# Optimization experiments

Measured on AMD Instinct MI355X. Metric: run time of the kernel, lower is better.

## Reference

```python
import jax, jax.numpy as jnp
import numpy as np

B, S, D = 4, 1024, 1024
H = 16
HD = D // H  # 64
NPOS = 64


def setup_inputs() -> dict:
    key = jax.random.key(0)
    ks = jax.random.split(key, 12)
    f = lambda k, shape, s=0.02: jax.random.normal(k, shape, dtype=jnp.float32) * s
    return {
        "q": jax.random.normal(ks[0], (B, S, D), dtype=jnp.float32),
        "k": jax.random.normal(ks[1], (B, S, D), dtype=jnp.float32),
        "v": jax.random.normal(ks[2], (B, S, D), dtype=jnp.float32),
        "Wq_w": f(ks[3], (D, D)), "Wq_b": f(ks[4], (D,)),
        "Wk_w": f(ks[5], (D, D)), "Wk_b": f(ks[6], (D,)),
        "Wv_w": f(ks[7], (D, D)), "Wv_b": f(ks[8], (D,)),
        "Wo_w": f(ks[9], (D, D)), "Wo_b": f(ks[10], (D,)),
        "pos_emb": f(ks[11], (HD, NPOS)),  # torch param is [1,1,head_dim,npos_max]
    }


def _proj(x, w, b):
    # nn.Linear: x @ w.T + b, then split heads -> [B, H, S, HD]
    y = jnp.einsum("bsd,ed->bse", x, w) + b
    bsz, s, _ = y.shape
    return y.reshape(bsz, s, H, HD).transpose(0, 2, 1, 3)


def reference(q, k, v, Wq_w, Wq_b, Wk_w, Wk_b, Wv_w, Wv_b, Wo_w, Wo_b, pos_emb):
    Q = _proj(q, Wq_w, Wq_b)
    K = _proj(k, Wk_w, Wk_b)
    V = _proj(v, Wv_w, Wv_b)

    scale = 1.0 / np.sqrt(HD).astype(np.float32)
    logits = jnp.einsum("bhqd,bhkd->bhqk", Q, K) * scale  # [B,H,S,S]

    # CoPE: sigmoid gates -> reverse cumsum -> interpolated position-logit gather
    gates = jax.nn.sigmoid(logits)
    pos = jnp.flip(jnp.cumsum(jnp.flip(gates, axis=-1), axis=-1), axis=-1)
    pos = jnp.minimum(pos, NPOS - 1)
    pos_floor = jnp.floor(pos)
    pos_ceil = jnp.ceil(pos)
    logits_int = jnp.einsum("bhqd,dn->bhqn", Q, pos_emb)  # [B,H,S,NPOS]
    lc = jnp.take_along_axis(logits_int, pos_ceil.astype(jnp.int32), axis=-1)
    lf = jnp.take_along_axis(logits_int, pos_floor.astype(jnp.int32), axis=-1)
    w = pos - pos_floor
    logits = logits + lc * w + lf * (1.0 - w)

    score = jax.nn.softmax(logits, axis=-1)
    out = jnp.einsum("bhqk,bhkd->bhqd", score, V)
    out = out.transpose(0, 2, 1, 3).reshape(q.shape[0], q.shape[1], D)
    return jnp.einsum("bsd,ed->bse", out, Wo_w) + Wo_b
```

## Files before the change

kernel.cpp:

```cpp
#include <hip/hip_runtime.h>
#include <hip/hip_bf16.h>

typedef __attribute__((ext_vector_type(8))) short short8;
typedef __attribute__((ext_vector_type(4))) short short4v;
typedef __attribute__((ext_vector_type(4))) float f32x4;
typedef unsigned short us;

#define MFMA16(a,b,c) __builtin_amdgcn_mfma_f32_16x16x32_bf16((a),(b),(c),0,0,0)

static __device__ __forceinline__ us bf16r(float x){
  unsigned u = __builtin_bit_cast(unsigned, x);
  u = u + 0x7fffu + ((u >> 16) & 1u);
  return (us)(u >> 16);
}
static __device__ __forceinline__ unsigned pk2(float a, float b){
  return (unsigned)bf16r(a) | ((unsigned)bf16r(b) << 16);
}

__global__ __launch_bounds__(256)
void castf2b(const float* __restrict__ in, us* __restrict__ out, int n){
  const int i = (blockIdx.x * 256 + threadIdx.x) * 4;
  if (i < n){
    const float4 v = *(const float4*)(in + i);
    short4v o;
    o[0] = (short)bf16r(v.x); o[1] = (short)bf16r(v.y);
    o[2] = (short)bf16r(v.z); o[3] = (short)bf16r(v.w);
    *(short4v*)(out + i) = o;
  }
}

__global__ __launch_bounds__(256)
void transpose_pe(const float* __restrict__ pe, us* __restrict__ peT){
  const int t = threadIdx.x;
  const int n = t & 63, dq = t >> 6;
#pragma unroll
  for (int j = 0; j < 16; ++j){
    const int d = dq * 16 + j;
    peT[n * 64 + d] = bf16r(pe[d * 64 + n]);
  }
}

__global__ __launch_bounds__(256)
void transpose_v(const us* __restrict__ Vb, us* __restrict__ VT){
  __shared__ __align__(16) us tile[64 * 72];
  const int t = threadIdx.x;
  const int stile = blockIdx.x & 15;
  const int bh = blockIdx.x >> 4;
  const int b = bh >> 4, h = bh & 15;
  const int s0 = stile << 6;
#pragma unroll
  for (int c = 0; c < 2; ++c){
    const int idx = t + (c << 8);
    const int sr = idx >> 3, cw = idx & 7;
    *(short8*)&tile[sr * 72 + cw * 8] =
        *(const short8*)(Vb + ((size_t)(b * 1024 + s0 + sr)) * 1024 + h * 64 + cw * 8);
  }
  __syncthreads();
#pragma unroll
  for (int c = 0; c < 2; ++c){
    const int idx = t + (c << 8);
    const int dr = idx >> 3, sw = idx & 7;
    short8 o;
#pragma unroll
    for (int j = 0; j < 8; ++j) o[j] = (short)tile[(sw * 8 + j) * 72 + dr];
    *(short8*)(VT + ((size_t)(bh * 64 + dr)) * 1024 + s0 + sw * 8) = o;
  }
}

template<bool OUT_BF16>
__global__ __launch_bounds__(256)
void gemm3_nt(const us* __restrict__ A0, const us* __restrict__ A1, const us* __restrict__ A2,
              const us* __restrict__ W0, const us* __restrict__ W1, const us* __restrict__ W2,
              const float* __restrict__ bp0, const float* __restrict__ bp1, const float* __restrict__ bp2,
              void* __restrict__ O0, void* __restrict__ O1, void* __restrict__ O2){
  __shared__ __align__(16) us Al[128 * 64];
  __shared__ __align__(16) us Bl[128 * 64];
  const int sel = blockIdx.y;
  const us* A      = sel == 0 ? A0 : (sel == 1 ? A1 : A2);
  const us* Wm     = sel == 0 ? W0 : (sel == 1 ? W1 : W2);
  const float* bias = sel == 0 ? bp0 : (sel == 1 ? bp1 : bp2);
  void* Ov         = sel == 0 ? O0 : (sel == 1 ? O1 : O2);
  const int tid = threadIdx.x;
  const int bm = blockIdx.x & 31, bn = blockIdx.x >> 5;
  const int m0 = bm << 7, n0 = bn << 7;
  const int w = tid >> 6, l = tid & 63;
  const int lr = l & 15, lg = l >> 4;
  const int wm = (w & 1) << 6, wn = (w >> 1) << 6;
  int srow[4], scol[4], sdst[4];
#pragma unroll
  for (int c = 0; c < 4; ++c){
    const int idx = tid + (c << 8);
    const int r = idx >> 3, cw = idx & 7;
    srow[c] = r; scol[c] = cw << 3;
    sdst[c] = r * 64 + ((cw << 3) ^ ((r & 7) << 3));
  }
  const int swz = (lr & 7) << 3;
  f32x4 acc[4][4];
#pragma unroll
  for (int i = 0; i < 4; ++i)
#pragma unroll
    for (int j = 0; j < 4; ++j) acc[i][j] = (f32x4){0.f, 0.f, 0.f, 0.f};

  short8 av[4], bv[4];
#pragma unroll
  for (int c = 0; c < 4; ++c){
    av[c] = *(const short8*)(A  + (size_t)(m0 + srow[c]) * 1024 + scol[c]);
    bv[c] = *(const short8*)(Wm + (size_t)(n0 + srow[c]) * 1024 + scol[c]);
  }
  for (int k0 = 0; k0 < 1024; k0 += 64){
    __syncthreads();
#pragma unroll
    for (int c = 0; c < 4; ++c){
      *(short8*)&Al[sdst[c]] = av[c];
      *(short8*)&Bl[sdst[c]] = bv[c];
    }
    __syncthreads();
    if (k0 < 960){
#pragma unroll
      for (int c = 0; c < 4; ++c){
        av[c] = *(const short8*)(A  + (size_t)(m0 + srow[c]) * 1024 + k0 + 64 + scol[c]);
        bv[c] = *(const short8*)(Wm + (size_t)(n0 + srow[c]) * 1024 + k0 + 64 + scol[c]);
      }
    }
#pragma unroll
    for (int ks = 0; ks < 2; ++ks){
      short8 af[4], bfv[4];
#pragma unroll
      for (int mt = 0; mt < 4; ++mt)
        af[mt] = *(const short8*)&Al[(wm + mt * 16 + lr) * 64 + (((ks << 5) + (lg << 3)) ^ swz)];
#pragma unroll
      for (int nt = 0; nt < 4; ++nt)
        bfv[nt] = *(const short8*)&Bl[(wn + nt * 16 + lr) * 64 + (((ks << 5) + (lg << 3)) ^ swz)];
#pragma unroll
      for (int mt = 0; mt < 4; ++mt)
#pragma unroll
        for (int nt = 0; nt < 4; ++nt)
          acc[mt][nt] = MFMA16(af[mt], bfv[nt], acc[mt][nt]);
    }
  }
  float bb[4];
#pragma unroll
  for (int nt = 0; nt < 4; ++nt) bb[nt] = bias[n0 + wn + nt * 16 + lr];
#pragma unroll
  for (int mt = 0; mt < 4; ++mt)
#pragma unroll
    for (int nt = 0; nt < 4; ++nt)
#pragma unroll
      for (int r = 0; r < 4; ++r){
        const size_t m = m0 + wm + mt * 16 + lg * 4 + r;
        const size_t n = n0 + wn + nt * 16 + lr;
        const float vv = acc[mt][nt][r] + bb[nt];
        if (OUT_BF16) ((us*)Ov)[m * 1024 + n] = bf16r(vv);
        else          ((float*)Ov)[m * 1024 + n] = vv;
      }
}

__global__ __launch_bounds__(256)
void cope_attn_mfma(const us* __restrict__ Qb, const us* __restrict__ Kb,
                    const us* __restrict__ VT, const us* __restrict__ peT,
                    us* __restrict__ Ob){
  __shared__ __align__(16) char smem[16 * 1028 * 4];
  __shared__ float li[16][68];
  float* logl = (float*)smem;
  const int tid = threadIdx.x;
  const int w = tid >> 6, l = tid & 63;
  const int lr = l & 15, lg = l >> 4;
  const int qt = blockIdx.x & 63;
  const int bh = blockIdx.x >> 6;
  const int b = bh >> 4, h = bh & 15;
  const int q0 = qt << 4;
  const us* Qh = Qb + ((size_t)(b * 1024 + q0)) * 1024 + h * 64;
  const us* Kh = Kb + ((size_t)(b * 1024)) * 1024 + h * 64;
  const us* Vh = VT + ((size_t)bh) * 64 * 1024;

  const short8 aq0 = *(const short8*)(Qh + (size_t)lr * 1024 + lg * 8);
  const short8 aq1 = *(const short8*)(Qh + (size_t)lr * 1024 + 32 + lg * 8);

  {
    f32x4 a = (f32x4){0.f, 0.f, 0.f, 0.f};
    const short8 p0 = *(const short8*)(peT + (size_t)(w * 16 + lr) * 64 + lg * 8);
    const short8 p1 = *(const short8*)(peT + (size_t)(w * 16 + lr) * 64 + 32 + lg * 8);
    a = MFMA16(aq0, p0, a);
    a = MFMA16(aq1, p1, a);
#pragma unroll
    for (int r = 0; r < 4; ++r) li[lg * 4 + r][w * 16 + lr] = a[r];
  }
  {
    const int kbase = w << 8;
    const us* Kw = Kh + (size_t)(kbase + lr) * 1024 + lg * 8;
    short8 b0 = *(const short8*)(Kw);
    short8 b1 = *(const short8*)(Kw + 32);
    for (int t = 0; t < 16; ++t){
      short8 n0v = b0, n1v = b1;
      if (t < 15){
        const us* Kn = Kw + (size_t)((t + 1) * 16) * 1024;
        n0v = *(const short8*)(Kn);
        n1v = *(const short8*)(Kn + 32);
      }
      f32x4 a = (f32x4){0.f, 0.f, 0.f, 0.f};
      a = MFMA16(aq0, b0, a);
      a = MFMA16(aq1, b1, a);
      const int kc = kbase + t * 16 + lr;
#pragma unroll
      for (int r = 0; r < 4; ++r) logl[(lg * 4 + r) * 1028 + kc] = a[r] * 0.125f;
      b0 = n0v; b1 = n1v;
    }
  }
  __syncthreads();
  unsigned pp[4][8];
#pragma unroll
  for (int rr = 0; rr < 4; ++rr){
    const int row = w * 4 + rr;
    const float* rowp = logl + row * 1028;
    f32x4 xv[4];
#pragma unroll
    for (int cb = 0; cb < 4; ++cb) xv[cb] = *(const f32x4*)(rowp + cb * 256 + l * 4);
    float s[4], pref[4][4];
#pragma unroll
    for (int cb = 0; cb < 4; ++cb){
      float run = 0.f;
#pragma unroll
      for (int j = 0; j < 4; ++j){
        const float g = 1.f / (1.f + __expf(-xv[cb][j]));
        pref[cb][j] = run;
        run += g;
      }
      s[cb] = run;
    }
    float T[4], lex[4];
#pragma unroll
    for (int cb = 0; cb < 4; ++cb){
      float run = s[cb];
#pragma unroll
      for (int off = 1; off < 64; off <<= 1){
        const float t2 = __shfl_up(run, off);
        if (l >= off) run += t2;
      }
      T[cb] = __shfl(run, 63);
      lex[cb] = run - s[cb];
    }
    float tt = 0.f, pb[4];
#pragma unroll
    for (int cb = 3; cb >= 0; --cb){ pb[cb] = tt + T[cb] - lex[cb]; tt += T[cb]; }
    float mx = -3.4e38f;
#pragma unroll
    for (int cb = 0; cb < 4; ++cb){
#pragma unroll
      for (int j = 0; j < 4; ++j){
        float p = pb[cb] - pref[cb][j];
        p = fminf(p, 63.f);
        p = fmaxf(p, 0.f);
        const float pf = floorf(p);
        const int il = (int)pf;
        const int ic = (int)ceilf(p);
        const float wt = p - pf;
        const float xx = xv[cb][j] + li[row][ic] * wt + li[row][il] * (1.f - wt);
        xv[cb][j] = xx;
        mx = fmaxf(mx, xx);
      }
    }
#pragma unroll
    for (int off = 1; off < 64; off <<= 1) mx = fmaxf(mx, __shfl_xor(mx, off));
    float sum = 0.f;
#pragma unroll
    for (int cb = 0; cb < 4; ++cb)
#pragma unroll
      for (int j = 0; j < 4; ++j){ const float e = __expf(xv[cb][j] - mx); xv[cb][j] = e; sum += e; }
#pragma unroll
    for (int off = 1; off < 64; off <<= 1) sum += __shfl_xor(sum, off);
    const float inv = 1.f / sum;
#pragma unroll
    for (int cb = 0; cb < 4; ++cb){
      pp[rr][cb * 2 + 0] = pk2(xv[cb][0] * inv, xv[cb][1] * inv);
      pp[rr][cb * 2 + 1] = pk2(xv[cb][2] * inv, xv[cb][3] * inv);
    }
  }
  __syncthreads();
  char* Pb = smem + 32768;
#pragma unroll
  for (int rr = 0; rr < 4; ++rr){
    const int row = w * 4 + rr;
#pragma unroll
    for (int cb = 0; cb < 4; ++cb){
      const int off = row * 2048 + ((cb * 512 + l * 8) ^ ((row & 7) << 4));
      uint2 vv; vv.x = pp[rr][cb * 2]; vv.y = pp[rr][cb * 2 + 1];
      *(uint2*)(Pb + off) = vv;
    }
  }
  __syncthreads();
  {
    const int d0 = w * 16;
    const int pswz = (lr & 7) << 4;
    f32x4 a = (f32x4){0.f, 0.f, 0.f, 0.f};
    const us* Vw = Vh + (size_t)(d0 + lr) * 1024 + lg * 8;
    short8 vb = *(const short8*)(Vw);
    for (int ks = 0; ks < 32; ++ks){
      short8 vn = vb;
      if (ks < 31) vn = *(const short8*)(Vw + (ks + 1) * 32);
      const short8 pa = *(const short8*)(Pb + lr * 2048 + (((ks << 6) + (lg << 4)) ^ pswz));
      a = MFMA16(pa, vb, a);
      vb = vn;
    }
#pragma unroll
    for (int r = 0; r < 4; ++r)
      Ob[((size_t)(b * 1024 + q0 + lg * 4 + r)) * 1024 + h * 64 + d0 + lr] = bf16r(a[r]);
  }
}

extern "C" void kernel_launch(void* const* d_in, const int* in_sizes, int n_in,
                              void* d_out, int out_size, void* d_ws, size_t ws_size,
                              hipStream_t stream) {
  const float* q    = (const float*)d_in[0];
  const float* k    = (const float*)d_in[1];
  const float* v    = (const float*)d_in[2];
  const float* Wq_w = (const float*)d_in[3];
  const float* Wq_b = (const float*)d_in[4];
  const float* Wk_w = (const float*)d_in[5];
  const float* Wk_b = (const float*)d_in[6];
  const float* Wv_w = (const float*)d_in[7];
  const float* Wv_b = (const float*)d_in[8];
  const float* Wo_w = (const float*)d_in[9];
  const float* Wo_b = (const float*)d_in[10];
  const float* pe   = (const float*)d_in[11];
  float* out = (float*)d_out;

  char* W = (char*)d_ws;
  const size_t MB = (size_t)1 << 20;
  us* qbf  = (us*)(W);
  us* kbf  = (us*)(W + 8 * MB);
  us* vbf  = (us*)(W + 16 * MB);
  us* Wqb  = (us*)(W + 24 * MB);
  us* Wkb  = (us*)(W + 26 * MB);
  us* Wvb  = (us*)(W + 28 * MB);
  us* Wob  = (us*)(W + 30 * MB);
  us* peTb = (us*)(W + 32 * MB);
  us* Qbf  = (us*)(W + 33 * MB);
  us* Kbf  = (us*)(W + 41 * MB);
  us* Vbf  = (us*)(W + 49 * MB);
  us* VTb  = qbf;
  us* Obf  = kbf;

  castf2b<<<4096, 256, 0, stream>>>(q, qbf, 4194304);
  castf2b<<<4096, 256, 0, stream>>>(k, kbf, 4194304);
  castf2b<<<4096, 256, 0, stream>>>(v, vbf, 4194304);
  castf2b<<<1024, 256, 0, stream>>>(Wq_w, Wqb, 1048576);
  castf2b<<<1024, 256, 0, stream>>>(Wk_w, Wkb, 1048576);
  castf2b<<<1024, 256, 0, stream>>>(Wv_w, Wvb, 1048576);
  castf2b<<<1024, 256, 0, stream>>>(Wo_w, Wob, 1048576);
  transpose_pe<<<1, 256, 0, stream>>>(pe, peTb);

  gemm3_nt<true><<<dim3(256, 3), 256, 0, stream>>>(
      qbf, kbf, vbf, Wqb, Wkb, Wvb, Wq_b, Wk_b, Wv_b, Qbf, Kbf, Vbf);
  transpose_v<<<1024, 256, 0, stream>>>(Vbf, VTb);
  cope_attn_mfma<<<4096, 256, 0, stream>>>(Qbf, Kbf, VTb, peTb, Obf);
  gemm3_nt<false><<<dim3(256, 1), 256, 0, stream>>>(
      Obf, Obf, Obf, Wob, Wob, Wob, Wo_b, Wo_b, Wo_b, out, out, out);
}
```

Measured before the change: 257.2 us.

## Fuse fp32-to-bf16 casts into GEMM loads and slim CoPE attention smem

Removes the seven separate cast kernels by converting fp32 inputs and weights to bf16 inside the GEMM global loads. The attention kernel now stores scaled logits as bf16 in a single swizzled shared buffer, reuses that buffer for the probabilities, and works in the log2 domain with raw v_exp/v_rcp instructions. Each lane handles 16 contiguous columns so a single prefix scan per row is enough. The smaller shared footprint allows more blocks per CU, at the cost of bf16 rounding of the logits before the sigmoid/cumsum, which may hurt accuracy.

```diff
diff --git a/kernel.cpp b/kernel.cpp
--- a/kernel.cpp
+++ b/kernel.cpp
@@ -2,11 +2,11 @@
 #include <hip/hip_bf16.h>
 
 typedef __attribute__((ext_vector_type(8))) short short8;
-typedef __attribute__((ext_vector_type(4))) short short4v;
 typedef __attribute__((ext_vector_type(4))) float f32x4;
 typedef unsigned short us;
 
 #define MFMA16(a,b,c) __builtin_amdgcn_mfma_f32_16x16x32_bf16((a),(b),(c),0,0,0)
+#define LOG2E 1.4426950408889634f
 
 static __device__ __forceinline__ us bf16r(float x){
   unsigned u = __builtin_bit_cast(unsigned, x);
@@ -16,17 +16,19 @@
 static __device__ __forceinline__ unsigned pk2(float a, float b){
   return (unsigned)bf16r(a) | ((unsigned)bf16r(b) << 16);
 }
-
-__global__ __launch_bounds__(256)
-void castf2b(const float* __restrict__ in, us* __restrict__ out, int n){
-  const int i = (blockIdx.x * 256 + threadIdx.x) * 4;
-  if (i < n){
-    const float4 v = *(const float4*)(in + i);
-    short4v o;
-    o[0] = (short)bf16r(v.x); o[1] = (short)bf16r(v.y);
-    o[2] = (short)bf16r(v.z); o[3] = (short)bf16r(v.w);
-    *(short4v*)(out + i) = o;
-  }
+static __device__ __forceinline__ short8 cvt8(float4 a, float4 b){
+  uint4 u; u.x = pk2(a.x, a.y); u.y = pk2(a.z, a.w);
+  u.z = pk2(b.x, b.y); u.w = pk2(b.z, b.w);
+  return __builtin_bit_cast(short8, u);
+}
+static __device__ __forceinline__ float b2f(us h){
+  return __builtin_bit_cast(float, (unsigned)h << 16);
+}
+static __device__ __forceinline__ float exp2fast(float x){
+  float r; asm("v_exp_f32 %0, %1" : "=v"(r) : "v"(x)); return r;
+}
+static __device__ __forceinline__ float rcpfast(float x){
+  float r; asm("v_rcp_f32 %0, %1" : "=v"(r) : "v"(x)); return r;
 }
 
 __global__ __launch_bounds__(256)
@@ -36,7 +38,7 @@
 #pragma unroll
   for (int j = 0; j < 16; ++j){
     const int d = dq * 16 + j;
-    peT[n * 64 + d] = bf16r(pe[d * 64 + n]);
+    peT[n * 64 + d] = bf16r(pe[d * 64 + n] * LOG2E);
   }
 }
 
@@ -67,19 +69,19 @@
   }
 }
 
-template<bool OUT_BF16>
+template<bool A_BF16, bool OUT_BF16>
 __global__ __launch_bounds__(256)
-void gemm3_nt(const us* __restrict__ A0, const us* __restrict__ A1, const us* __restrict__ A2,
-              const us* __restrict__ W0, const us* __restrict__ W1, const us* __restrict__ W2,
-              const float* __restrict__ bp0, const float* __restrict__ bp1, const float* __restrict__ bp2,
-              void* __restrict__ O0, void* __restrict__ O1, void* __restrict__ O2){
+void gemm3(const void* __restrict__ Av0, const void* __restrict__ Av1, const void* __restrict__ Av2,
+           const float* __restrict__ W0, const float* __restrict__ W1, const float* __restrict__ W2,
+           const float* __restrict__ bp0, const float* __restrict__ bp1, const float* __restrict__ bp2,
+           void* __restrict__ O0, void* __restrict__ O1, void* __restrict__ O2){
   __shared__ __align__(16) us Al[128 * 64];
   __shared__ __align__(16) us Bl[128 * 64];
   const int sel = blockIdx.y;
-  const us* A      = sel == 0 ? A0 : (sel == 1 ? A1 : A2);
-  const us* Wm     = sel == 0 ? W0 : (sel == 1 ? W1 : W2);
+  const void* Av   = sel == 0 ? Av0 : (sel == 1 ? Av1 : Av2);
+  const float* Wm  = sel == 0 ? W0  : (sel == 1 ? W1  : W2);
   const float* bias = sel == 0 ? bp0 : (sel == 1 ? bp1 : bp2);
-  void* Ov         = sel == 0 ? O0 : (sel == 1 ? O1 : O2);
+  void* Ov         = sel == 0 ? O0  : (sel == 1 ? O1  : O2);
   const int tid = threadIdx.x;
   const int bm = blockIdx.x & 31, bn = blockIdx.x >> 5;
   const int m0 = bm << 7, n0 = bn << 7;
@@ -101,12 +103,23 @@
 #pragma unroll
     for (int j = 0; j < 4; ++j) acc[i][j] = (f32x4){0.f, 0.f, 0.f, 0.f};
 
+  auto ldA = [&](int c, int k) -> short8 {
+    if constexpr (A_BF16){
+      return *(const short8*)((const us*)Av + (size_t)(m0 + srow[c]) * 1024 + k + scol[c]);
+    } else {
+      const float* p = (const float*)Av + (size_t)(m0 + srow[c]) * 1024 + k + scol[c];
+      return cvt8(*(const float4*)p, *(const float4*)(p + 4));
+    }
+  };
+  auto ldW = [&](int c, int k) -> short8 {
+    const float* p = Wm + (size_t)(n0 + srow[c]) * 1024 + k + scol[c];
+    return cvt8(*(const float4*)p, *(const float4*)(p + 4));
+  };
+
   short8 av[4], bv[4];
 #pragma unroll
-  for (int c = 0; c < 4; ++c){
-    av[c] = *(const short8*)(A  + (size_t)(m0 + srow[c]) * 1024 + scol[c]);
-    bv[c] = *(const short8*)(Wm + (size_t)(n0 + srow[c]) * 1024 + scol[c]);
-  }
+  for (int c = 0; c < 4; ++c){ av[c] = ldA(c, 0); bv[c] = ldW(c, 0); }
+
   for (int k0 = 0; k0 < 1024; k0 += 64){
     __syncthreads();
 #pragma unroll
@@ -117,10 +130,7 @@
     __syncthreads();
     if (k0 < 960){
 #pragma unroll
-      for (int c = 0; c < 4; ++c){
-        av[c] = *(const short8*)(A  + (size_t)(m0 + srow[c]) * 1024 + k0 + 64 + scol[c]);
-        bv[c] = *(const short8*)(Wm + (size_t)(n0 + srow[c]) * 1024 + k0 + 64 + scol[c]);
-      }
+      for (int c = 0; c < 4; ++c){ av[c] = ldA(c, k0 + 64); bv[c] = ldW(c, k0 + 64); }
     }
 #pragma unroll
     for (int ks = 0; ks < 2; ++ks){
@@ -155,13 +165,12 @@
       }
 }
 
-__global__ __launch_bounds__(256)
-void cope_attn_mfma(const us* __restrict__ Qb, const us* __restrict__ Kb,
-                    const us* __restrict__ VT, const us* __restrict__ peT,
-                    us* __restrict__ Ob){
-  __shared__ __align__(16) char smem[16 * 1028 * 4];
-  __shared__ float li[16][68];
-  float* logl = (float*)smem;
+__global__ __launch_bounds__(256, 4)
+void cope_attn_v3(const us* __restrict__ Qb, const us* __restrict__ Kb,
+                  const us* __restrict__ VT, const us* __restrict__ peT,
+                  us* __restrict__ Ob){
+  __shared__ __align__(16) us yl[16 * 1024];
+  __shared__ float li2[16][68];
   const int tid = threadIdx.x;
   const int w = tid >> 6, l = tid & 63;
   const int lr = l & 15, lg = l >> 4;
@@ -172,6 +181,7 @@
   const us* Qh = Qb + ((size_t)(b * 1024 + q0)) * 1024 + h * 64;
   const us* Kh = Kb + ((size_t)(b * 1024)) * 1024 + h * 64;
   const us* Vh = VT + ((size_t)bh) * 64 * 1024;
+  const float QSC = 0.125f * LOG2E;
 
   const short8 aq0 = *(const short8*)(Qh + (size_t)lr * 1024 + lg * 8);
   const short8 aq1 = *(const short8*)(Qh + (size_t)lr * 1024 + 32 + lg * 8);
@@ -183,7 +193,7 @@
     a = MFMA16(aq0, p0, a);
     a = MFMA16(aq1, p1, a);
 #pragma unroll
-    for (int r = 0; r < 4; ++r) li[lg * 4 + r][w * 16 + lr] = a[r];
+    for (int r = 0; r < 4; ++r) li2[lg * 4 + r][w * 16 + lr] = a[r];
   }
   {
     const int kbase = w << 8;
@@ -200,104 +210,84 @@
       f32x4 a = (f32x4){0.f, 0.f, 0.f, 0.f};
       a = MFMA16(aq0, b0, a);
       a = MFMA16(aq1, b1, a);
-      const int kc = kbase + t * 16 + lr;
-#pragma unroll
-      for (int r = 0; r < 4; ++r) logl[(lg * 4 + r) * 1028 + kc] = a[r] * 0.125f;
+#pragma unroll
+      for (int r = 0; r < 4; ++r){
+        const int row = lg * 4 + r;
+        const int kc = kbase + t * 16 + lr;
+        yl[row * 1024 + (((kc >> 3) ^ (row & 7)) << 3) + (kc & 7)] = bf16r(a[r] * QSC);
+      }
       b0 = n0v; b1 = n1v;
     }
   }
   __syncthreads();
-  unsigned pp[4][8];
 #pragma unroll
   for (int rr = 0; rr < 4; ++rr){
     const int row = w * 4 + rr;
-    const float* rowp = logl + row * 1028;
-    f32x4 xv[4];
-#pragma unroll
-    for (int cb = 0; cb < 4; ++cb) xv[cb] = *(const f32x4*)(rowp + cb * 256 + l * 4);
-    float s[4], pref[4][4];
-#pragma unroll
-    for (int cb = 0; cb < 4; ++cb){
-      float run = 0.f;
-#pragma unroll
-      for (int j = 0; j < 4; ++j){
-        const float g = 1.f / (1.f + __expf(-xv[cb][j]));
-        pref[cb][j] = run;
-        run += g;
-      }
-      s[cb] = run;
-    }
-    float T[4], lex[4];
-#pragma unroll
-    for (int cb = 0; cb < 4; ++cb){
-      float run = s[cb];
-#pragma unroll
-      for (int off = 1; off < 64; off <<= 1){
-        const float t2 = __shfl_up(run, off);
-        if (l >= off) run += t2;
-      }
-      T[cb] = __shfl(run, 63);
-      lex[cb] = run - s[cb];
-    }
-    float tt = 0.f, pb[4];
-#pragma unroll
-    for (int cb = 3; cb >= 0; --cb){ pb[cb] = tt + T[cb] - lex[cb]; tt += T[cb]; }
+    const int sz = row & 7;
+    const int ad0 = row * 1024 + (((2 * l) ^ sz) << 3);
+    const int ad1 = row * 1024 + (((2 * l + 1) ^ sz) << 3);
+    const short8 y0 = *(const short8*)&yl[ad0];
+    const short8 y1 = *(const short8*)&yl[ad1];
+    float x[16];
+#pragma unroll
+    for (int j = 0; j < 8; ++j){ x[j] = b2f((us)y0[j]); x[8 + j] = b2f((us)y1[j]); }
+    float pref[16];
+    float s = 0.f;
+#pragma unroll
+    for (int i = 0; i < 16; ++i){
+      const float g = rcpfast(1.f + exp2fast(-x[i]));
+      pref[i] = s;
+      s += g;
+    }
+    float run = s;
+#pragma unroll
+    for (int off = 1; off < 64; off <<= 1){
+      const float t2 = __shfl_up(run, off);
+      if (l >= off) run += t2;
+    }
+    const float T = __shfl(run, 63);
+    const float base = T - (run - s);
     float mx = -3.4e38f;
 #pragma unroll
-    for (int cb = 0; cb < 4; ++cb){
-#pragma unroll
-      for (int j = 0; j < 4; ++j){
-        float p = pb[cb] - pref[cb][j];
-        p = fminf(p, 63.f);
-        p = fmaxf(p, 0.f);
-        const float pf = floorf(p);
-        const int il = (int)pf;
-        const int ic = (int)ceilf(p);
-        const float wt = p - pf;
-        const float xx = xv[cb][j] + li[row][ic] * wt + li[row][il] * (1.f - wt);
-        xv[cb][j] = xx;
-        mx = fmaxf(mx, xx);
-      }
+    for (int i = 0; i < 16; ++i){
+      float p = base - pref[i];
+      p = fminf(p, 63.f);
+      p = fmaxf(p, 0.f);
+      const float pf = floorf(p);
+      const int il = (int)pf;
+      const int ic = (int)ceilf(p);
+      const float wt = p - pf;
+      const float xx = x[i] + li2[row][ic] * wt + li2[row][il] * (1.f - wt);
+      x[i] = xx;
+      mx = fmaxf(mx, xx);
     }
 #pragma unroll
     for (int off = 1; off < 64; off <<= 1) mx = fmaxf(mx, __shfl_xor(mx, off));
     float sum = 0.f;
 #pragma unroll
-    for (int cb = 0; cb < 4; ++cb)
-#pragma unroll
-      for (int j = 0; j < 4; ++j){ const float e = __expf(xv[cb][j] - mx); xv[cb][j] = e; sum += e; }
+    for (int i = 0; i < 16; ++i){ const float e = exp2fast(x[i] - mx); x[i] = e; sum += e; }
 #pragma unroll
     for (int off = 1; off < 64; off <<= 1) sum += __shfl_xor(sum, off);
-    const float inv = 1.f / sum;
-#pragma unroll
-    for (int cb = 0; cb < 4; ++cb){
-      pp[rr][cb * 2 + 0] = pk2(xv[cb][0] * inv, xv[cb][1] * inv);
-      pp[rr][cb * 2 + 1] = pk2(xv[cb][2] * inv, xv[cb][3] * inv);
-    }
-  }
-  __syncthreads();
-  char* Pb = smem + 32768;
-#pragma unroll
-  for (int rr = 0; rr < 4; ++rr){
-    const int row = w * 4 + rr;
-#pragma unroll
-    for (int cb = 0; cb < 4; ++cb){
-      const int off = row * 2048 + ((cb * 512 + l * 8) ^ ((row & 7) << 4));
-      uint2 vv; vv.x = pp[rr][cb * 2]; vv.y = pp[rr][cb * 2 + 1];
-      *(uint2*)(Pb + off) = vv;
-    }
+    const float inv = rcpfast(sum);
+    uint4 ua, ub;
+    ua.x = pk2(x[0] * inv,  x[1] * inv);  ua.y = pk2(x[2] * inv,  x[3] * inv);
+    ua.z = pk2(x[4] * inv,  x[5] * inv);  ua.w = pk2(x[6] * inv,  x[7] * inv);
+    ub.x = pk2(x[8] * inv,  x[9] * inv);  ub.y = pk2(x[10] * inv, x[11] * inv);
+    ub.z = pk2(x[12] * inv, x[13] * inv); ub.w = pk2(x[14] * inv, x[15] * inv);
+    *(uint4*)&yl[ad0] = ua;
+    *(uint4*)&yl[ad1] = ub;
   }
   __syncthreads();
   {
     const int d0 = w * 16;
-    const int pswz = (lr & 7) << 4;
+    const int psw = lr & 7;
     f32x4 a = (f32x4){0.f, 0.f, 0.f, 0.f};
     const us* Vw = Vh + (size_t)(d0 + lr) * 1024 + lg * 8;
     short8 vb = *(const short8*)(Vw);
     for (int ks = 0; ks < 32; ++ks){
       short8 vn = vb;
       if (ks < 31) vn = *(const short8*)(Vw + (ks + 1) * 32);
-      const short8 pa = *(const short8*)(Pb + lr * 2048 + (((ks << 6) + (lg << 4)) ^ pswz));
+      const short8 pa = *(const short8*)&yl[lr * 1024 + ((((ks << 2) + lg) ^ psw) << 3)];
       a = MFMA16(pa, vb, a);
       vb = vn;
     }
@@ -326,33 +316,18 @@
 
   char* W = (char*)d_ws;
   const size_t MB = (size_t)1 << 20;
-  us* qbf  = (us*)(W);
-  us* kbf  = (us*)(W + 8 * MB);
-  us* vbf  = (us*)(W + 16 * MB);
-  us* Wqb  = (us*)(W + 24 * MB);
-  us* Wkb  = (us*)(W + 26 * MB);
-  us* Wvb  = (us*)(W + 28 * MB);
-  us* Wob  = (us*)(W + 30 * MB);
-  us* peTb = (us*)(W + 32 * MB);
-  us* Qbf  = (us*)(W + 33 * MB);
-  us* Kbf  = (us*)(W + 41 * MB);
-  us* Vbf  = (us*)(W + 49 * MB);
-  us* VTb  = qbf;
-  us* Obf  = kbf;
-
-  castf2b<<<4096, 256, 0, stream>>>(q, qbf, 4194304);
-  castf2b<<<4096, 256, 0, stream>>>(k, kbf, 4194304);
-  castf2b<<<4096, 256, 0, stream>>>(v, vbf, 4194304);
-  castf2b<<<1024, 256, 0, stream>>>(Wq_w, Wqb, 1048576);
-  castf2b<<<1024, 256, 0, stream>>>(Wk_w, Wkb, 1048576);
-  castf2b<<<1024, 256, 0, stream>>>(Wv_w, Wvb, 1048576);
-  castf2b<<<1024, 256, 0, stream>>>(Wo_w, Wob, 1048576);
-  transpose_pe<<<1, 256, 0, stream>>>(pe, peTb);
-
-  gemm3_nt<true><<<dim3(256, 3), 256, 0, stream>>>(
-      qbf, kbf, vbf, Wqb, Wkb, Wvb, Wq_b, Wk_b, Wv_b, Qbf, Kbf, Vbf);
+  us* Qbf = (us*)(W);
+  us* Kbf = (us*)(W + 8 * MB);
+  us* Vbf = (us*)(W + 16 * MB);
+  us* VTb = (us*)(W + 24 * MB);
+  us* Obf = (us*)(W + 32 * MB);
+  us* peT = (us*)(W + 40 * MB);
+
+  transpose_pe<<<1, 256, 0, stream>>>(pe, peT);
+  gemm3<false, true><<<dim3(256, 3), 256, 0, stream>>>(
+      q, k, v, Wq_w, Wk_w, Wv_w, Wq_b, Wk_b, Wv_b, Qbf, Kbf, Vbf);
   transpose_v<<<1024, 256, 0, stream>>>(Vbf, VTb);
-  cope_attn_mfma<<<4096, 256, 0, stream>>>(Qbf, Kbf, VTb, peTb, Obf);
-  gemm3_nt<false><<<dim3(256, 1), 256, 0, stream>>>(
-      Obf, Obf, Obf, Wob, Wob, Wob, Wo_b, Wo_b, Wo_b, out, out, out);
-}
+  cope_attn_v3<<<4096, 256, 0, stream>>>(Qbf, Kbf, VTb, peT, Obf);
+  gemm3<true, false><<<dim3(256, 1), 256, 0, stream>>>(
+      Obf, Obf, Obf, Wo_w, Wo_w, Wo_w, Wo_b, Wo_b, Wo_b, out, out, out);
+}
```

New measurement: 220.5 us. 1.17x faster.
